# Kernel optimization log

Hardware: AMD Instinct MI355X
Metric: run time of the kernel (lower is better)

## Reference

```python
import jax, jax.numpy as jnp
import numpy as np

B, H, HKV, S, D = 1, 32, 4, 2048, 128
NEG = -1e9  # causal mask fill (float32-safe, like torch finfo.min in spirit)


def setup_inputs() -> dict:
    key = jax.random.key(0)
    kq, kk, kv, ks = jax.random.split(key, 4)
    query = jax.random.normal(kq, (B, H, S, D), dtype=jnp.float32)
    k = jax.random.normal(kk, (B, HKV, S, D), dtype=jnp.float32)
    v = jax.random.normal(kv, (B, HKV, S, D), dtype=jnp.float32)
    sinks = jax.random.normal(ks, (H,), dtype=jnp.float32)
    # causal additive mask [B, 1, S, S]
    causal = jnp.where(jnp.tril(jnp.ones((S, S), dtype=bool)), 0.0, NEG).astype(jnp.float32)
    attention_mask = jnp.broadcast_to(causal[None, None], (B, 1, S, S))
    return {"query": query, "key": k, "value": v,
            "attention_mask": attention_mask, "sinks": sinks}


def reference(query, key, value, attention_mask, sinks):
    scaling = 1.0 / jnp.sqrt(jnp.asarray(D, dtype=query.dtype))
    groups = H // HKV
    # repeat_kv: [B, HKV, S, D] -> [B, H, S, D]
    k = jnp.repeat(key, groups, axis=1)
    v = jnp.repeat(value, groups, axis=1)
    # scores [B, H, S, S]
    attn = jnp.einsum('bhqd,bhkd->bhqk', query, k) * scaling
    attn = attn + attention_mask[:, :, :, :attn.shape[-1]]
    # append per-head sink column -> [B, H, S, S+1]
    sink_col = jnp.broadcast_to(sinks.reshape(1, H, 1, 1), (B, H, S, 1)).astype(attn.dtype)
    combined = jnp.concatenate([attn, sink_col], axis=-1)
    combined = combined - jnp.max(combined, axis=-1, keepdims=True)
    probs = jax.nn.softmax(combined, axis=-1)[..., :-1]
    # PV matmul, then [B, H, S, D] -> [B, S, H, D]
    out = jnp.einsum('bhqk,bhkd->bhqd', probs, v)
    return jnp.transpose(out, (0, 2, 1, 3))
```

## Files before the change

### kernel.cpp

```cpp
#include <hip/hip_runtime.h>
#include <hip/hip_bf16.h>


#define NH    32
#define SEQ   2048
#define HD    128
#define KVB   64
#define KTILE 16384
#define KVHB  (32 * KTILE)

typedef __attribute__((ext_vector_type(8)))  short bf16x8;
typedef __attribute__((ext_vector_type(4)))  float f32x4;
typedef __attribute__((ext_vector_type(16))) float f32x16;

#define LGKM0  asm volatile("s_waitcnt lgkmcnt(0)" ::: "memory")
#define VMCNT0 asm volatile("s_waitcnt vmcnt(0)" ::: "memory")

static __device__ __forceinline__ unsigned short f2bf(float f) {
  __hip_bfloat16 h = __float2bfloat16(f);
  union { __hip_bfloat16 h; unsigned short u; } c; c.h = h;
  return c.u;
}
static __device__ __forceinline__ unsigned int pk2(float a, float b) {
  return (unsigned int)f2bf(a) | ((unsigned int)f2bf(b) << 16);
}
static __device__ __forceinline__ bf16x8 mk8(unsigned int w0, unsigned int w1,
                                             unsigned int w2, unsigned int w3) {
  union { unsigned int w[4]; bf16x8 v; } t;
  t.w[0] = w0; t.w[1] = w1; t.w[2] = w2; t.w[3] = w3; return t.v;
}

__global__ __launch_bounds__(256)
void convert_kv(const float* __restrict__ K, const float* __restrict__ V,
                char* __restrict__ Ki, char* __restrict__ Vi)
{
  const int b = blockIdx.x;
  const float* Ks = K + (size_t)b * (KVB * HD);
  const float* Vs = V + (size_t)b * (KVB * HD);
  char* kt = Ki + (size_t)b * KTILE;
  char* vt = Vi + (size_t)b * KTILE;
  const int tid   = threadIdx.x;
  const int r16   = tid >> 4;
  const int dcol  = (tid & 15) * 8;
  const int dstep = dcol >> 4;
  const int h2d   = (dcol >> 3) & 1;
  #pragma unroll
  for (int i = 0; i < 4; ++i) {
    const int row = i * 16 + r16;
    float tk[8], tv[8];
    *(f32x4*)(tk)     = *(const f32x4*)(Ks + row * HD + dcol);
    *(f32x4*)(tk + 4) = *(const f32x4*)(Ks + row * HD + dcol + 4);
    *(f32x4*)(tv)     = *(const f32x4*)(Vs + row * HD + dcol);
    *(f32x4*)(tv + 4) = *(const f32x4*)(Vs + row * HD + dcol + 4);
    bf16x8 k8;
    #pragma unroll
    for (int j = 0; j < 8; ++j) k8[j] = (short)f2bf(tk[j]);
    *(bf16x8*)(kt + ((row >> 5) * 8 + dstep) * 1024 + (h2d * 32 + (row & 31)) * 16) = k8;
    const int s = (row >> 4) & 3, h2v = (row >> 3) & 1, jv = row & 7;
    #pragma unroll
    for (int j = 0; j < 8; ++j) {
      const int d = dcol + j;
      *(unsigned short*)(vt + ((d >> 5) * 4 + s) * 1024 + (h2v * 32 + (d & 31)) * 16 + jv * 2)
        = f2bf(tv[j]);
    }
  }
}

__device__ __forceinline__ void stage2(const char* kimg, const char* vimg,
                                       char* kb, char* vb, int tid) {
  #pragma unroll
  for (int k = 0; k < 4; ++k)
    __builtin_amdgcn_global_load_lds((const unsigned int*)(kimg + k * 4096 + tid * 16),
                                     (unsigned int*)(kb + k * 4096 + tid * 16), 16, 0, 0);
  #pragma unroll
  for (int k = 0; k < 4; ++k)
    __builtin_amdgcn_global_load_lds((const unsigned int*)(vimg + k * 4096 + tid * 16),
                                     (unsigned int*)(vb + k * 4096 + tid * 16), 16, 0, 0);
}

__global__ __launch_bounds__(256, 2)
void attn_fwd(const float* __restrict__ Q, const float* __restrict__ sinks,
              const char* __restrict__ Ki, const char* __restrict__ Vi,
              float* __restrict__ out)
{
  __shared__ __align__(16) char KB[2][16384];
  __shared__ __align__(16) char VB[2][16384];
  __shared__ float sml[2][32];

  const int tid  = threadIdx.x;
  const int lane = tid & 63;
  const int w    = tid >> 6;
  const int qs   = w >> 1;
  const int ws   = w & 1;
  const int lq   = lane & 31;
  const int hi   = lane >> 5;

  const int bid = blockIdx.x;
  const int h   = bid >> 4;
  const int j   = bid & 15;
  const int kvh = h >> 3;

  const char* Kt = Ki + (size_t)kvh * KVHB;
  const char* Vt = Vi + (size_t)kvh * KVHB;

  const float QSC = 0.08838834764831845f * 1.4426950408889634f;
  const float EC  = 17.312340490667562f;
  const float sadd = __builtin_amdgcn_exp2f(sinks[h] * 1.4426950408889634f - EC);

  int cur = 0;
  stage2(Kt, Vt, KB[0], VB[0], tid);

  #pragma unroll 1
  for (int su = 0; su < 2; ++su) {
    const int qt = su ? j : (31 - j);
    const int q0 = qt * 64;
    const int nt = qt + 1;
    const int qb = q0 + qs * 32;
    const int qme = qb + lq;

    bf16x8 qf[8];
    {
      const float* qp = Q + ((size_t)h * SEQ + qme) * HD + hi * 8;
      #pragma unroll
      for (int dstep = 0; dstep < 8; ++dstep) {
        float t0[8];
        *(f32x4*)(t0)     = *(const f32x4*)(qp + dstep * 16);
        *(f32x4*)(t0 + 4) = *(const f32x4*)(qp + dstep * 16 + 4);
        bf16x8 qv;
        #pragma unroll
        for (int jj = 0; jj < 8; ++jj) qv[jj] = (short)f2bf(t0[jj] * QSC);
        qf[dstep] = qv;
      }
    }

    f32x16 acc[4];
    #pragma unroll
    for (int d = 0; d < 4; ++d)
      acc[d] = (f32x16){0.f,0.f,0.f,0.f,0.f,0.f,0.f,0.f,0.f,0.f,0.f,0.f,0.f,0.f,0.f,0.f};
    float lsum = 0.f;

    for (int i = 0; i < nt; ++i) {
      LGKM0; VMCNT0;
      __builtin_amdgcn_s_barrier();
      if (i + 1 < nt)
        stage2(Kt + (size_t)(i + 1) * KTILE,
               Vt + (size_t)(i + 1) * KTILE, KB[cur ^ 1], VB[cur ^ 1], tid);
      else if (su == 0)
        stage2(Kt, Vt, KB[cur ^ 1], VB[cur ^ 1], tid);

      const int kv0 = i * KVB + ws * 32;
      if (kv0 <= qb + 31) {
        const char* kb = KB[cur] + ws * 8192 + lane * 16;
        const char* vb = VB[cur] + lane * 16;

        f32x16 sc = (f32x16){0.f,0.f,0.f,0.f,0.f,0.f,0.f,0.f,0.f,0.f,0.f,0.f,0.f,0.f,0.f,0.f};
        #pragma unroll
        for (int dstep = 0; dstep < 8; ++dstep) {
          bf16x8 kf = *(const bf16x8*)(kb + dstep * 1024);
          sc = __builtin_amdgcn_mfma_f32_32x32x16_bf16(kf, qf[dstep], sc, 0, 0, 0);
        }

        float p[16];
        #pragma unroll
        for (int r = 0; r < 16; ++r)
          p[r] = __builtin_amdgcn_exp2f(sc[r] - EC);
        if (kv0 + 31 > qb) {
          const int kvbase = kv0 + 4 * hi;
          #pragma unroll
          for (int r = 0; r < 16; ++r) {
            const int kv = kvbase + (r & 3) + 8 * (r >> 2);
            if (kv > qme) p[r] = 0.f;
          }
        }
        #pragma unroll
        for (int r = 0; r < 16; ++r) lsum += p[r];

        unsigned int X0 = pk2(p[0],  p[1]),  X1 = pk2(p[2],  p[3]);
        unsigned int Y0 = pk2(p[4],  p[5]),  Y1 = pk2(p[6],  p[7]);
        unsigned int Z0 = pk2(p[8],  p[9]),  Z1 = pk2(p[10], p[11]);
        unsigned int W0 = pk2(p[12], p[13]), W1 = pk2(p[14], p[15]);
        asm volatile("v_permlane32_swap_b32 %0, %1" : "+v"(X0), "+v"(Y0));
        asm volatile("v_permlane32_swap_b32 %0, %1" : "+v"(X1), "+v"(Y1));
        asm volatile("v_permlane32_swap_b32 %0, %1" : "+v"(Z0), "+v"(W0));
        asm volatile("v_permlane32_swap_b32 %0, %1" : "+v"(Z1), "+v"(W1));
        bf16x8 pf0 = mk8(X0, X1, Y0, Y1);
        bf16x8 pf1 = mk8(Z0, Z1, W0, W1);

        #pragma unroll
        for (int dblk = 0; dblk < 4; ++dblk) {
          bf16x8 vf0 = *(const bf16x8*)(vb + (dblk * 4 + ws * 2 + 0) * 1024);
          bf16x8 vf1 = *(const bf16x8*)(vb + (dblk * 4 + ws * 2 + 1) * 1024);
          acc[dblk] = __builtin_amdgcn_mfma_f32_32x32x16_bf16(vf0, pf0, acc[dblk], 0, 0, 0);
          acc[dblk] = __builtin_amdgcn_mfma_f32_32x32x16_bf16(vf1, pf1, acc[dblk], 0, 0, 0);
        }
      }
      cur ^= 1;
    }

    lsum += __shfl_xor(lsum, 32);
    char* scratch = (qs == 0) ? KB[cur ^ 1] : VB[cur ^ 1];
    LGKM0; VMCNT0;
    __builtin_amdgcn_s_barrier();
    if (ws == 1) {
      #pragma unroll
      for (int dblk = 0; dblk < 4; ++dblk)
        #pragma unroll
        for (int m = 0; m < 4; ++m) {
          f32x4 t;
          #pragma unroll
          for (int e = 0; e < 4; ++e) t[e] = acc[dblk][4 * m + e];
          *(f32x4*)(scratch + lq * 512 +
                    ((dblk * 128 + m * 32 + hi * 16) ^ ((lq & 7) << 4))) = t;
        }
      if (lane < 32) sml[qs][lq] = lsum;
    }
    LGKM0;
    __builtin_amdgcn_s_barrier();
    if (ws == 0) {
      #pragma unroll
      for (int dblk = 0; dblk < 4; ++dblk)
        #pragma unroll
        for (int m = 0; m < 4; ++m) {
          f32x4 t = *(const f32x4*)(scratch + lq * 512 +
                     ((dblk * 128 + m * 32 + hi * 16) ^ ((lq & 7) << 4)));
          #pragma unroll
          for (int e = 0; e < 4; ++e) acc[dblk][4 * m + e] += t[e];
        }
      LGKM0;
      const float rd = 1.0f / (lsum + sml[qs][lq] + sadd);

      const int qrow = lane >> 1;
      const int half = lane & 1;
      const int sx   = qrow & 7;
      #pragma unroll
      for (int dblk = 0; dblk < 4; ++dblk) {
        #pragma unroll
        for (int m = 0; m < 4; ++m) {
          f32x4 t;
          #pragma unroll
          for (int e = 0; e < 4; ++e) t[e] = acc[dblk][4 * m + e] * rd;
          *(f32x4*)(scratch + lq * 128 + ((m * 32 + hi * 16) ^ ((lq & 7) << 4))) = t;
        }
        LGKM0;
        float* og = out + (((size_t)(qb + qrow)) * NH + h) * HD + dblk * 32 + half * 16;
        #pragma unroll
        for (int c = 0; c < 4; ++c) {
          f32x4 t = *(const f32x4*)(scratch + qrow * 128 + (((half * 4 + c) ^ sx) * 16));
          *(f32x4*)(og + c * 4) = t;
        }
        LGKM0;
      }
    }
  }
}

extern "C" void kernel_launch(void* const* d_in, const int* in_sizes, int n_in,
                              void* d_out, int out_size, void* d_ws, size_t ws_size,
                              hipStream_t stream) {
  const float* Q     = (const float*)d_in[0];
  const float* K     = (const float*)d_in[1];
  const float* V     = (const float*)d_in[2];
  const float* sinks = (const float*)d_in[4];
  float* out = (float*)d_out;

  char* Ki = (char*)d_ws;
  char* Vi = Ki + (size_t)4 * KVHB;

  convert_kv<<<dim3(128), 256, 0, stream>>>(K, V, Ki, Vi);
  attn_fwd<<<dim3(512), 256, 0, stream>>>(Q, sinks, Ki, Vi, out);
}
```

Before: 75.43 us.

## Load V fragments directly from global, halve LDS, raise occupancy to 3 blocks

V tiles are no longer staged through LDS. Each wave reads its V fragments straight from global memory into registers before the QK MFMAs, and only K stays double-buffered via global_load_lds. With LDS use halved, launch bounds rise to 3 blocks per CU. Block-to-head mapping is reordered so blocks sharing a KV head launch together for L2 reuse, and MFMA sections get s_setprio. The epilogue now serializes the two q-subtile reductions through a single K scratch buffer, which adds barriers and raises register pressure under the tighter launch bound.

```diff
diff --git a/kernel.cpp b/kernel.cpp
--- a/kernel.cpp
+++ b/kernel.cpp
@@ -1,6 +1,5 @@
 #include <hip/hip_runtime.h>
 #include <hip/hip_bf16.h>
-
 
 #define NH    32
 #define SEQ   2048
@@ -66,25 +65,19 @@
   }
 }
 
-__device__ __forceinline__ void stage2(const char* kimg, const char* vimg,
-                                       char* kb, char* vb, int tid) {
+__device__ __forceinline__ void stageK(const char* kimg, char* kb, int tid) {
   #pragma unroll
   for (int k = 0; k < 4; ++k)
     __builtin_amdgcn_global_load_lds((const unsigned int*)(kimg + k * 4096 + tid * 16),
                                      (unsigned int*)(kb + k * 4096 + tid * 16), 16, 0, 0);
-  #pragma unroll
-  for (int k = 0; k < 4; ++k)
-    __builtin_amdgcn_global_load_lds((const unsigned int*)(vimg + k * 4096 + tid * 16),
-                                     (unsigned int*)(vb + k * 4096 + tid * 16), 16, 0, 0);
-}
-
-__global__ __launch_bounds__(256, 2)
+}
+
+__global__ __launch_bounds__(256, 3)
 void attn_fwd(const float* __restrict__ Q, const float* __restrict__ sinks,
               const char* __restrict__ Ki, const char* __restrict__ Vi,
               float* __restrict__ out)
 {
   __shared__ __align__(16) char KB[2][16384];
-  __shared__ __align__(16) char VB[2][16384];
   __shared__ float sml[2][32];
 
   const int tid  = threadIdx.x;
@@ -96,9 +89,10 @@
   const int hi   = lane >> 5;
 
   const int bid = blockIdx.x;
-  const int h   = bid >> 4;
-  const int j   = bid & 15;
-  const int kvh = h >> 3;
+  const int p   = bid & 31;
+  const int j   = bid >> 5;
+  const int kvh = (p & 7) >> 1;
+  const int h   = kvh * 8 + (p >> 3) * 2 + (p & 1);
 
   const char* Kt = Ki + (size_t)kvh * KVHB;
   const char* Vt = Vi + (size_t)kvh * KVHB;
@@ -107,9 +101,9 @@
   const float EC  = 17.312340490667562f;
   const float sadd = __builtin_amdgcn_exp2f(sinks[h] * 1.4426950408889634f - EC);
 
-  int cur = 0;
-  stage2(Kt, Vt, KB[0], VB[0], tid);
-
+  stageK(Kt, KB[0], tid);
+
+  int gbase = 0;
   #pragma unroll 1
   for (int su = 0; su < 2; ++su) {
     const int qt = su ? j : (31 - j);
@@ -140,45 +134,56 @@
     float lsum = 0.f;
 
     for (int i = 0; i < nt; ++i) {
-      LGKM0; VMCNT0;
+      const int g = gbase + i;
+      VMCNT0;
       __builtin_amdgcn_s_barrier();
-      if (i + 1 < nt)
-        stage2(Kt + (size_t)(i + 1) * KTILE,
-               Vt + (size_t)(i + 1) * KTILE, KB[cur ^ 1], VB[cur ^ 1], tid);
-      else if (su == 0)
-        stage2(Kt, Vt, KB[cur ^ 1], VB[cur ^ 1], tid);
 
       const int kv0 = i * KVB + ws * 32;
-      if (kv0 <= qb + 31) {
-        const char* kb = KB[cur] + ws * 8192 + lane * 16;
-        const char* vb = VB[cur] + lane * 16;
-
-        f32x16 sc = (f32x16){0.f,0.f,0.f,0.f,0.f,0.f,0.f,0.f,0.f,0.f,0.f,0.f,0.f,0.f,0.f,0.f};
+      const bool act = (kv0 <= qb + 31);
+
+      bf16x8 vf[8];
+      if (act) {
+        const char* vg = Vt + (size_t)i * KTILE + lane * 16;
+        #pragma unroll
+        for (int f8 = 0; f8 < 8; ++f8) {
+          const int dblk = f8 >> 1, sdx = f8 & 1;
+          vf[f8] = *(const bf16x8*)(vg + (dblk * 4 + ws * 2 + sdx) * 1024);
+        }
+      }
+
+      if (i + 1 < nt)       stageK(Kt + (size_t)(i + 1) * KTILE, KB[(g + 1) & 1], tid);
+      else if (su == 0)     stageK(Kt, KB[(g + 1) & 1], tid);
+
+      if (act) {
+        const char* kb = KB[g & 1] + ws * 8192 + lane * 16;
+        f32x16 sc = (f32x16){0.f,0.f,0.f,0.f,0.f,0.f,0.f,0.f,
+                             0.f,0.f,0.f,0.f,0.f,0.f,0.f,0.f};
+        __builtin_amdgcn_s_setprio(1);
         #pragma unroll
         for (int dstep = 0; dstep < 8; ++dstep) {
           bf16x8 kf = *(const bf16x8*)(kb + dstep * 1024);
           sc = __builtin_amdgcn_mfma_f32_32x32x16_bf16(kf, qf[dstep], sc, 0, 0, 0);
         }
-
-        float p[16];
+        __builtin_amdgcn_s_setprio(0);
+
+        float pp[16];
         #pragma unroll
         for (int r = 0; r < 16; ++r)
-          p[r] = __builtin_amdgcn_exp2f(sc[r] - EC);
+          pp[r] = __builtin_amdgcn_exp2f(sc[r] - EC);
         if (kv0 + 31 > qb) {
           const int kvbase = kv0 + 4 * hi;
           #pragma unroll
           for (int r = 0; r < 16; ++r) {
             const int kv = kvbase + (r & 3) + 8 * (r >> 2);
-            if (kv > qme) p[r] = 0.f;
-          }
-        }
-        #pragma unroll
-        for (int r = 0; r < 16; ++r) lsum += p[r];
-
-        unsigned int X0 = pk2(p[0],  p[1]),  X1 = pk2(p[2],  p[3]);
-        unsigned int Y0 = pk2(p[4],  p[5]),  Y1 = pk2(p[6],  p[7]);
-        unsigned int Z0 = pk2(p[8],  p[9]),  Z1 = pk2(p[10], p[11]);
-        unsigned int W0 = pk2(p[12], p[13]), W1 = pk2(p[14], p[15]);
+            if (kv > qme) pp[r] = 0.f;
+          }
+        }
+        #pragma unroll
+        for (int r = 0; r < 16; ++r) lsum += pp[r];
+        unsigned int X0 = pk2(pp[0],  pp[1]),  X1 = pk2(pp[2],  pp[3]);
+        unsigned int Y0 = pk2(pp[4],  pp[5]),  Y1 = pk2(pp[6],  pp[7]);
+        unsigned int Z0 = pk2(pp[8],  pp[9]),  Z1 = pk2(pp[10], pp[11]);
+        unsigned int W0 = pk2(pp[12], pp[13]), W1 = pk2(pp[14], pp[15]);
         asm volatile("v_permlane32_swap_b32 %0, %1" : "+v"(X0), "+v"(Y0));
         asm volatile("v_permlane32_swap_b32 %0, %1" : "+v"(X1), "+v"(Y1));
         asm volatile("v_permlane32_swap_b32 %0, %1" : "+v"(Z0), "+v"(W0));
@@ -186,71 +191,77 @@
         bf16x8 pf0 = mk8(X0, X1, Y0, Y1);
         bf16x8 pf1 = mk8(Z0, Z1, W0, W1);
 
+        __builtin_amdgcn_s_setprio(1);
         #pragma unroll
         for (int dblk = 0; dblk < 4; ++dblk) {
-          bf16x8 vf0 = *(const bf16x8*)(vb + (dblk * 4 + ws * 2 + 0) * 1024);
-          bf16x8 vf1 = *(const bf16x8*)(vb + (dblk * 4 + ws * 2 + 1) * 1024);
-          acc[dblk] = __builtin_amdgcn_mfma_f32_32x32x16_bf16(vf0, pf0, acc[dblk], 0, 0, 0);
-          acc[dblk] = __builtin_amdgcn_mfma_f32_32x32x16_bf16(vf1, pf1, acc[dblk], 0, 0, 0);
-        }
-      }
-      cur ^= 1;
-    }
-
+          acc[dblk] = __builtin_amdgcn_mfma_f32_32x32x16_bf16(vf[2 * dblk + 0], pf0, acc[dblk], 0, 0, 0);
+          acc[dblk] = __builtin_amdgcn_mfma_f32_32x32x16_bf16(vf[2 * dblk + 1], pf1, acc[dblk], 0, 0, 0);
+        }
+        __builtin_amdgcn_s_setprio(0);
+      }
+    }
+
+    const int gnext = gbase + nt;
+    char* scratch = (char*)KB[(gnext & 1) ^ 1];
     lsum += __shfl_xor(lsum, 32);
-    char* scratch = (qs == 0) ? KB[cur ^ 1] : VB[cur ^ 1];
     LGKM0; VMCNT0;
     __builtin_amdgcn_s_barrier();
-    if (ws == 1) {
-      #pragma unroll
-      for (int dblk = 0; dblk < 4; ++dblk)
-        #pragma unroll
-        for (int m = 0; m < 4; ++m) {
-          f32x4 t;
-          #pragma unroll
-          for (int e = 0; e < 4; ++e) t[e] = acc[dblk][4 * m + e];
-          *(f32x4*)(scratch + lq * 512 +
-                    ((dblk * 128 + m * 32 + hi * 16) ^ ((lq & 7) << 4))) = t;
-        }
-      if (lane < 32) sml[qs][lq] = lsum;
-    }
-    LGKM0;
-    __builtin_amdgcn_s_barrier();
-    if (ws == 0) {
-      #pragma unroll
-      for (int dblk = 0; dblk < 4; ++dblk)
-        #pragma unroll
-        for (int m = 0; m < 4; ++m) {
-          f32x4 t = *(const f32x4*)(scratch + lq * 512 +
-                     ((dblk * 128 + m * 32 + hi * 16) ^ ((lq & 7) << 4)));
-          #pragma unroll
-          for (int e = 0; e < 4; ++e) acc[dblk][4 * m + e] += t[e];
-        }
+    #pragma unroll 1
+    for (int rq = 0; rq < 2; ++rq) {
+      if (qs == rq && ws == 1) {
+        #pragma unroll
+        for (int dblk = 0; dblk < 4; ++dblk)
+          #pragma unroll
+          for (int m = 0; m < 4; ++m) {
+            f32x4 t;
+            #pragma unroll
+            for (int e = 0; e < 4; ++e) t[e] = acc[dblk][4 * m + e];
+            *(f32x4*)(scratch + lq * 512 +
+                      ((dblk * 128 + m * 32 + hi * 16) ^ ((lq & 7) << 4))) = t;
+          }
+        if (lane < 32) sml[rq][lq] = lsum;
+      }
       LGKM0;
-      const float rd = 1.0f / (lsum + sml[qs][lq] + sadd);
-
-      const int qrow = lane >> 1;
-      const int half = lane & 1;
-      const int sx   = qrow & 7;
-      #pragma unroll
-      for (int dblk = 0; dblk < 4; ++dblk) {
-        #pragma unroll
-        for (int m = 0; m < 4; ++m) {
-          f32x4 t;
-          #pragma unroll
-          for (int e = 0; e < 4; ++e) t[e] = acc[dblk][4 * m + e] * rd;
-          *(f32x4*)(scratch + lq * 128 + ((m * 32 + hi * 16) ^ ((lq & 7) << 4))) = t;
-        }
+      __builtin_amdgcn_s_barrier();
+      if (qs == rq && ws == 0) {
+        #pragma unroll
+        for (int dblk = 0; dblk < 4; ++dblk)
+          #pragma unroll
+          for (int m = 0; m < 4; ++m) {
+            f32x4 t = *(const f32x4*)(scratch + lq * 512 +
+                       ((dblk * 128 + m * 32 + hi * 16) ^ ((lq & 7) << 4)));
+            #pragma unroll
+            for (int e = 0; e < 4; ++e) acc[dblk][4 * m + e] += t[e];
+          }
         LGKM0;
-        float* og = out + (((size_t)(qb + qrow)) * NH + h) * HD + dblk * 32 + half * 16;
-        #pragma unroll
-        for (int c = 0; c < 4; ++c) {
-          f32x4 t = *(const f32x4*)(scratch + qrow * 128 + (((half * 4 + c) ^ sx) * 16));
-          *(f32x4*)(og + c * 4) = t;
-        }
-        LGKM0;
-      }
-    }
+        const float rd = 1.0f / (lsum + sml[rq][lq] + sadd);
+
+        const int qrow = lane >> 1;
+        const int half = lane & 1;
+        const int sx   = qrow & 7;
+        #pragma unroll
+        for (int dblk = 0; dblk < 4; ++dblk) {
+          #pragma unroll
+          for (int m = 0; m < 4; ++m) {
+            f32x4 t;
+            #pragma unroll
+            for (int e = 0; e < 4; ++e) t[e] = acc[dblk][4 * m + e] * rd;
+            *(f32x4*)(scratch + lq * 128 + ((m * 32 + hi * 16) ^ ((lq & 7) << 4))) = t;
+          }
+          LGKM0;
+          float* og = out + (((size_t)(qb + qrow)) * NH + h) * HD + dblk * 32 + half * 16;
+          #pragma unroll
+          for (int c = 0; c < 4; ++c) {
+            f32x4 t = *(const f32x4*)(scratch + qrow * 128 + (((half * 4 + c) ^ sx) * 16));
+            *(f32x4*)(og + c * 4) = t;
+          }
+          LGKM0;
+        }
+      }
+      LGKM0;
+      __builtin_amdgcn_s_barrier();
+    }
+    gbase = gnext;
   }
 }
 
```

After: 114.1 us. 51.3% more time.
